# Kernel tuning notes

Hardware: AMD Instinct MI355X
Metric: run time of the kernel (lower is better)

The kernel has to match this reference:

```python
import jax, jax.numpy as jnp
import numpy as np

B, N_SRC, N_TGT = 2, 2048, 2048
DIM, HEADS, DIM_HEAD, DIM_ROT = 1024, 16, 64, 32
INNER = HEADS * DIM_HEAD
SCALE = DIM_HEAD ** -0.5


def rotate_every_two(x):
    # (..., d) with d even: pairs (x1, x2) -> (-x2, x1), interleaved
    x1 = x[..., ::2]
    x2 = x[..., 1::2]
    return jnp.stack((-x2, x1), axis=-1).reshape(x.shape)


def setup_inputs() -> dict:
    key = jax.random.key(0)
    ks = jax.random.split(key, 10)
    return {
        "src": jax.random.normal(ks[0], (B, N_SRC, DIM), jnp.float32),
        "sin_src": jax.random.uniform(ks[1], (B, N_SRC, DIM_ROT), jnp.float32, -1.0, 1.0),
        "cos_src": jax.random.uniform(ks[2], (B, N_SRC, DIM_ROT), jnp.float32, -1.0, 1.0),
        "tgt": jax.random.normal(ks[3], (B, N_TGT, DIM), jnp.float32),
        "sin_tgt": jax.random.uniform(ks[4], (B, N_TGT, DIM_ROT), jnp.float32, -1.0, 1.0),
        "cos_tgt": jax.random.uniform(ks[5], (B, N_TGT, DIM_ROT), jnp.float32, -1.0, 1.0),
        "wq": jax.random.normal(ks[6], (DIM, INNER), jnp.float32) / np.sqrt(DIM),
        "wkv": jax.random.normal(ks[7], (DIM, 2 * INNER), jnp.float32) / np.sqrt(DIM),
        "wout": jax.random.normal(ks[8], (INNER, DIM), jnp.float32) / np.sqrt(INNER),
        "bout": jnp.zeros((DIM,), jnp.float32),
    }


def reference(src, sin_src, cos_src, tgt, sin_tgt, cos_tgt, wq, wkv, wout, bout):
    b = src.shape[0]
    q = tgt @ wq                                  # (b, i, inner)
    k, v = jnp.split(src @ wkv, 2, axis=-1)       # (b, j, inner) each

    def split_heads(t):
        return t.reshape(b, t.shape[1], HEADS, DIM_HEAD).transpose(0, 2, 1, 3)

    q, k, v = map(split_heads, (q, k, v))          # (b, h, n, d)

    # rotary on leading DIM_ROT dims; pos embs broadcast across heads
    st, ct = sin_tgt[:, None], cos_tgt[:, None]    # (b, 1, i, dr)
    ss, cs = sin_src[:, None], cos_src[:, None]    # (b, 1, j, dr)
    q_rot, q_pass = q[..., :DIM_ROT], q[..., DIM_ROT:]
    k_rot, k_pass = k[..., :DIM_ROT], k[..., DIM_ROT:]
    q_rot = q_rot * ct + rotate_every_two(q_rot) * st
    k_rot = k_rot * cs + rotate_every_two(k_rot) * ss
    q = jnp.concatenate([q_rot, q_pass], axis=-1)
    k = jnp.concatenate([k_rot, k_pass], axis=-1)

    dots = jnp.einsum('bhid,bhjd->bhij', q, k) * SCALE
    attn = jax.nn.softmax(dots, axis=-1)
    out = jnp.einsum('bhij,bhjd->bhid', attn, v)
    out = out.transpose(0, 2, 1, 3).reshape(b, out.shape[2], INNER)
    return out @ wout + bout, attn
```

## Files before the change

kernel.cpp:

```cpp
#include <hip/hip_runtime.h>
#include <hip/hip_bf16.h>
#include <cstdint>
#include <cstddef>

#define NB 2
#define NSEQ 2048
#define NHEADS 16
#define HD 64
#define DMODEL 1024
#define SCALEF 0.125f

typedef __attribute__((ext_vector_type(4))) float f32x4;
typedef __attribute__((ext_vector_type(8))) short s16x8;

__device__ __forceinline__ unsigned short f2bf(float f) {
  union { float f; unsigned u; } v; v.f = f;
  unsigned u = v.u;
  return (unsigned short)((u + 0x7fffu + ((u >> 16) & 1u)) >> 16);
}
__device__ __forceinline__ float bf2f(unsigned short s) {
  union { unsigned u; float f; } v; v.u = ((unsigned)s) << 16;
  return v.f;
}

__global__ void k_convert(const float* __restrict__ in, unsigned short* __restrict__ out, int n4) {
  int i = blockIdx.x * blockDim.x + threadIdx.x;
  if (i >= n4) return;
  float4 v = ((const float4*)in)[i];
  ushort4 o;
  o.x = f2bf(v.x); o.y = f2bf(v.y); o.z = f2bf(v.z); o.w = f2bf(v.w);
  ((ushort4*)out)[i] = o;
}

__global__ void k_transpose(const float* __restrict__ w, unsigned short* __restrict__ wt, int K, int N) {
  __shared__ float t[64][65];
  int n0 = blockIdx.x * 64, k0 = blockIdx.y * 64;
  int c = threadIdx.x & 63, rb = threadIdx.x >> 6;
#pragma unroll
  for (int rr = 0; rr < 16; rr++) {
    int k = rb * 16 + rr;
    t[c][k] = w[(size_t)(k0 + k) * N + n0 + c];
  }
  __syncthreads();
#pragma unroll
  for (int rr = 0; rr < 16; rr++) {
    int n = rb * 16 + rr;
    wt[(size_t)(n0 + n) * K + k0 + c] = f2bf(t[n][c]);
  }
}

#define GLD16(gp, lp) __builtin_amdgcn_global_load_lds( \
    (const __attribute__((address_space(1))) unsigned int*)(gp), \
    (__attribute__((address_space(3))) unsigned int*)(lp), 16, 0, 0)

__global__ __launch_bounds__(256) void k_gemm(const unsigned short* __restrict__ A,
                                              const unsigned short* __restrict__ Bt,
                                              float* __restrict__ C,
                                              const float* __restrict__ bias,
                                              int M, int N, int K) {
  __shared__ unsigned short As[128 * 32];
  __shared__ unsigned short Bs[128 * 32];
  const int tid = threadIdx.x;
  const int lane = tid & 63, wid = tid >> 6;
  const int m0 = blockIdx.y * 128, n0 = blockIdx.x * 128;
  const int wr = wid >> 1, wc = wid & 1;
  const int lr = lane >> 2, l4 = lane & 3;
  const int lc = lane & 15, lg = lane >> 4;

  const unsigned short* pa0 = A + (size_t)(m0 + wid * 32 + lr) * K + l4 * 8;
  const unsigned short* pa1 = pa0 + (size_t)16 * K;
  const unsigned short* pb0 = Bt + (size_t)(n0 + wid * 32 + lr) * K + l4 * 8;
  const unsigned short* pb1 = pb0 + (size_t)16 * K;

  f32x4 acc[4][4] = {};

  for (int kt = 0; kt < K; kt += 32) {
    GLD16(pa0 + kt, &As[wid * 1024]);
    GLD16(pa1 + kt, &As[wid * 1024 + 512]);
    GLD16(pb0 + kt, &Bs[wid * 1024]);
    GLD16(pb1 + kt, &Bs[wid * 1024 + 512]);
    __syncthreads();
    s16x8 af[4], bfr[4];
#pragma unroll
    for (int m = 0; m < 4; m++)
      af[m] = *(const s16x8*)&As[(wr * 64 + m * 16 + lc) * 32 + lg * 8];
#pragma unroll
    for (int n = 0; n < 4; n++)
      bfr[n] = *(const s16x8*)&Bs[(wc * 64 + n * 16 + lc) * 32 + lg * 8];
    __builtin_amdgcn_s_setprio(1);
#pragma unroll
    for (int m = 0; m < 4; m++)
#pragma unroll
      for (int n = 0; n < 4; n++)
        acc[m][n] = __builtin_amdgcn_mfma_f32_16x16x32_bf16(af[m], bfr[n], acc[m][n], 0, 0, 0);
    __builtin_amdgcn_s_setprio(0);
    __syncthreads();
  }

  float bv[4] = {0.f, 0.f, 0.f, 0.f};
  if (bias) {
#pragma unroll
    for (int n = 0; n < 4; n++) bv[n] = bias[n0 + wc * 64 + n * 16 + lc];
  }
#pragma unroll
  for (int m = 0; m < 4; m++) {
#pragma unroll
    for (int n = 0; n < 4; n++) {
      int col = n0 + wc * 64 + n * 16 + lc;
#pragma unroll
      for (int r = 0; r < 4; r++) {
        int row = m0 + wr * 64 + m * 16 + lg * 4 + r;
        C[(size_t)row * N + col] = acc[m][n][r] + bv[n];
      }
    }
  }
}

__global__ void k_rope(const float* __restrict__ src, int row_stride,
                       const float* __restrict__ sinp, const float* __restrict__ cosp,
                       unsigned short* __restrict__ dst) {
  int tid = blockIdx.x * 256 + threadIdx.x;
  int p = tid & 31;
  int h = (tid >> 5) & 15;
  int i = (tid >> 9) & 2047;
  int b = tid >> 20;
  int d = p * 2;
  float2 x = *(const float2*)(src + (size_t)(b * NSEQ + i) * row_stride + h * HD + d);
  float o0, o1;
  if (p < 16) {
    size_t sc = (size_t)(b * NSEQ + i) * 32 + d;
    float2 cc = *(const float2*)(cosp + sc);
    float2 ss = *(const float2*)(sinp + sc);
    o0 = x.x * cc.x - x.y * ss.x;
    o1 = x.y * cc.y + x.x * ss.y;
  } else { o0 = x.x; o1 = x.y; }
  size_t off = ((size_t)(b * NHEADS + h) * NSEQ + i) * HD + d;
  unsigned pack = (unsigned)f2bf(o0) | ((unsigned)f2bf(o1) << 16);
  *(unsigned*)(dst + off) = pack;
}

__global__ void k_vtrans(const float* __restrict__ kv, unsigned short* __restrict__ vt) {
  __shared__ float t[64][65];
  int i0 = blockIdx.x * 64;
  int h = blockIdx.y, b = blockIdx.z;
  int c = threadIdx.x & 63, rb = threadIdx.x >> 6;
#pragma unroll
  for (int rr = 0; rr < 16; rr++) {
    int il = rb * 16 + rr;
    t[il][c] = kv[(size_t)(b * NSEQ + i0 + il) * 2048 + 1024 + h * HD + c];
  }
  __syncthreads();
#pragma unroll
  for (int rr = 0; rr < 16; rr++) {
    int dd = rb * 16 + rr;
    vt[((size_t)(b * NHEADS + h) * HD + dd) * NSEQ + i0 + c] = f2bf(t[c][dd]);
  }
}

#define QBLK 32
#define SROWB 2056
__global__ __launch_bounds__(1024, 4) void k_attn(const unsigned short* __restrict__ qh,
                                                  const unsigned short* __restrict__ kh,
                                                  const unsigned short* __restrict__ vt,
                                                  float* __restrict__ attn_g,
                                                  unsigned short* __restrict__ ctx) {
  __shared__ unsigned short Sbf[QBLK * SROWB];
  __shared__ float wred[16][32];
  __shared__ float invr[32];
  float* part = (float*)Sbf;

  const int tid = threadIdx.x;
  const int lane = tid & 63, wid = tid >> 6;
  const int i0 = blockIdx.x * QBLK;
  const int h = blockIdx.y, b = blockIdx.z;
  const int lc = lane & 15, lg = lane >> 4;
  const int wcb = wid * 128;

  const unsigned short* qb = qh + ((size_t)(b * NHEADS + h) * NSEQ + i0) * HD;
  const unsigned short* kb = kh + (size_t)(b * NHEADS + h) * NSEQ * HD;
  const unsigned short* vb = vt + (size_t)(b * NHEADS + h) * HD * NSEQ;

  s16x8 aq[2][2];
#pragma unroll
  for (int rg = 0; rg < 2; rg++) {
    aq[rg][0] = *(const s16x8*)&qb[(rg * 16 + lc) * HD + lg * 8];
    aq[rg][1] = *(const s16x8*)&qb[(rg * 16 + lc) * HD + 32 + lg * 8];
  }
  float psum[2][4] = {};
  const unsigned short* krow = kb + (size_t)(wcb + lc) * HD + lg * 8;
  s16x8 kp[2][2];
  kp[0][0] = *(const s16x8*)&krow[0];
  kp[0][1] = *(const s16x8*)&krow[32];
#pragma unroll
  for (int jf = 0; jf < 8; jf++) {
    if (jf < 7) {
      kp[(jf + 1) & 1][0] = *(const s16x8*)&krow[(size_t)((jf + 1) * 16) * HD];
      kp[(jf + 1) & 1][1] = *(const s16x8*)&krow[(size_t)((jf + 1) * 16) * HD + 32];
    }
    int j = wcb + jf * 16;
#pragma unroll
    for (int rg = 0; rg < 2; rg++) {
      f32x4 acc = {};
      acc = __builtin_amdgcn_mfma_f32_16x16x32_bf16(aq[rg][0], kp[jf & 1][0], acc, 0, 0, 0);
      acc = __builtin_amdgcn_mfma_f32_16x16x32_bf16(aq[rg][1], kp[jf & 1][1], acc, 0, 0, 0);
#pragma unroll
      for (int r = 0; r < 4; r++) {
        float e = __expf(acc[r] * SCALEF);
        psum[rg][r] += e;
        Sbf[(size_t)(rg * 16 + lg * 4 + r) * SROWB + j + lc] = f2bf(e);
      }
    }
  }
#pragma unroll
  for (int off = 1; off <= 8; off <<= 1)
#pragma unroll
    for (int rg = 0; rg < 2; rg++)
#pragma unroll
      for (int r = 0; r < 4; r++) psum[rg][r] += __shfl_xor(psum[rg][r], off);
  if (lc == 0) {
#pragma unroll
    for (int rg = 0; rg < 2; rg++)
#pragma unroll
      for (int r = 0; r < 4; r++) wred[wid][rg * 16 + lg * 4 + r] = psum[rg][r];
  }
  __syncthreads();
  if (tid < 32) {
    float tot = 0.f;
#pragma unroll
    for (int w = 0; w < 16; w++) tot += wred[w][tid];
    invr[tid] = 1.0f / tot;
  }

  f32x4 accd[2][4] = {};
  const unsigned short* vrow = vb + (size_t)lc * NSEQ + wcb + lg * 8;
  s16x8 vp[2][4];
#pragma unroll
  for (int f = 0; f < 4; f++)
    vp[0][f] = *(const s16x8*)&vrow[(size_t)(f * 16) * NSEQ];
#pragma unroll
  for (int jj = 0; jj < 4; jj++) {
    if (jj < 3) {
#pragma unroll
      for (int f = 0; f < 4; f++)
        vp[(jj + 1) & 1][f] = *(const s16x8*)&vrow[(size_t)(f * 16) * NSEQ + (jj + 1) * 32];
    }
    int jb = wcb + jj * 32;
    s16x8 af0 = *(const s16x8*)&Sbf[(size_t)lc * SROWB + jb + lg * 8];
    __builtin_amdgcn_s_setprio(1);
#pragma unroll
    for (int f = 0; f < 4; f++)
      accd[0][f] = __builtin_amdgcn_mfma_f32_16x16x32_bf16(af0, vp[jj & 1][f], accd[0][f], 0, 0, 0);
    __builtin_amdgcn_s_setprio(0);
    s16x8 af1 = *(const s16x8*)&Sbf[(size_t)(16 + lc) * SROWB + jb + lg * 8];
    __builtin_amdgcn_s_setprio(1);
#pragma unroll
    for (int f = 0; f < 4; f++)
      accd[1][f] = __builtin_amdgcn_mfma_f32_16x16x32_bf16(af1, vp[jj & 1][f], accd[1][f], 0, 0, 0);
    __builtin_amdgcn_s_setprio(0);
  }
  __syncthreads();

  {
    const int srow = tid >> 5;
    const int scc = (tid & 31) * 8;
    const float inv = invr[srow];
    float* arow = attn_g + ((size_t)(b * NHEADS + h) * NSEQ + i0 + srow) * NSEQ + scc;
#pragma unroll
    for (int k = 0; k < 8; k++) {
      s16x8 ev = *(const s16x8*)&Sbf[(size_t)srow * SROWB + scc + k * 256];
      f32x4 f0, f1;
      f0[0] = bf2f((unsigned short)ev[0]) * inv;
      f0[1] = bf2f((unsigned short)ev[1]) * inv;
      f0[2] = bf2f((unsigned short)ev[2]) * inv;
      f0[3] = bf2f((unsigned short)ev[3]) * inv;
      f1[0] = bf2f((unsigned short)ev[4]) * inv;
      f1[1] = bf2f((unsigned short)ev[5]) * inv;
      f1[2] = bf2f((unsigned short)ev[6]) * inv;
      f1[3] = bf2f((unsigned short)ev[7]) * inv;
      *(f32x4*)&arow[k * 256] = f0;
      *(f32x4*)&arow[k * 256 + 4] = f1;
    }
  }
  __syncthreads();

  if (wid < 8) {
#pragma unroll
    for (int rg = 0; rg < 2; rg++)
#pragma unroll
      for (int f = 0; f < 4; f++)
#pragma unroll
        for (int r = 0; r < 4; r++)
          part[((size_t)wid * 32 + rg * 16 + lg * 4 + r) * 65 + f * 16 + lc] = accd[rg][f][r];
  }
  __syncthreads();
  if (wid >= 8) {
#pragma unroll
    for (int rg = 0; rg < 2; rg++)
#pragma unroll
      for (int f = 0; f < 4; f++)
#pragma unroll
        for (int r = 0; r < 4; r++)
          part[((size_t)(wid - 8) * 32 + rg * 16 + lg * 4 + r) * 65 + f * 16 + lc] += accd[rg][f][r];
  }
  __syncthreads();

  {
    const int oi = tid >> 5;
    const int d0 = (tid & 31) * 2;
    float s0 = 0.f, s1 = 0.f;
#pragma unroll
    for (int p = 0; p < 8; p++) {
      s0 += part[((size_t)p * 32 + oi) * 65 + d0];
      s1 += part[((size_t)p * 32 + oi) * 65 + d0 + 1];
    }
    float iv = invr[oi];
    ushort2 o;
    o.x = f2bf(s0 * iv);
    o.y = f2bf(s1 * iv);
    *(ushort2*)&ctx[(size_t)(b * NSEQ + i0 + oi) * DMODEL + h * HD + d0] = o;
  }
}

extern "C" void kernel_launch(void* const* d_in, const int* in_sizes, int n_in,
                              void* d_out, int out_size, void* d_ws, size_t ws_size,
                              hipStream_t stream) {
  const float* src     = (const float*)d_in[0];
  const float* sin_src = (const float*)d_in[1];
  const float* cos_src = (const float*)d_in[2];
  const float* tgt     = (const float*)d_in[3];
  const float* sin_tgt = (const float*)d_in[4];
  const float* cos_tgt = (const float*)d_in[5];
  const float* wq      = (const float*)d_in[6];
  const float* wkv     = (const float*)d_in[7];
  const float* wout    = (const float*)d_in[8];
  const float* bout    = (const float*)d_in[9];

  if (ws_size < (size_t)109051904) return;

  uint8_t* w = (uint8_t*)d_ws;
  unsigned short* tgt_bf = (unsigned short*)(w + 0);
  unsigned short* src_bf = (unsigned short*)(w + 8388608);
  unsigned short* wq_t   = (unsigned short*)(w + 16777216);
  unsigned short* wkv_t  = (unsigned short*)(w + 18874368);
  unsigned short* wout_t = (unsigned short*)(w + 23068672);
  float*          q_ws   = (float*)(w + 25165824);
  float*          kv_ws  = (float*)(w + 41943040);
  unsigned short* qhb    = (unsigned short*)(w + 75497472);
  unsigned short* khb    = (unsigned short*)(w + 83886080);
  unsigned short* vtb    = (unsigned short*)(w + 92274688);
  unsigned short* ctx    = (unsigned short*)(w + 100663296);

  float* out_p  = (float*)d_out;
  float* attn_p = out_p + (size_t)NB * NSEQ * DMODEL;

  k_convert<<<4096, 256, 0, stream>>>(tgt, tgt_bf, 1048576);
  k_convert<<<4096, 256, 0, stream>>>(src, src_bf, 1048576);
  k_transpose<<<dim3(16, 16), 256, 0, stream>>>(wq,   wq_t,   1024, 1024);
  k_transpose<<<dim3(32, 16), 256, 0, stream>>>(wkv,  wkv_t,  1024, 2048);
  k_transpose<<<dim3(16, 16), 256, 0, stream>>>(wout, wout_t, 1024, 1024);

  k_gemm<<<dim3(8, 32),  256, 0, stream>>>(tgt_bf, wq_t,  q_ws,  nullptr, 4096, 1024, 1024);
  k_gemm<<<dim3(16, 32), 256, 0, stream>>>(src_bf, wkv_t, kv_ws, nullptr, 4096, 2048, 1024);

  k_rope<<<8192, 256, 0, stream>>>(q_ws, 1024, sin_tgt, cos_tgt, qhb);
  k_rope<<<8192, 256, 0, stream>>>(kv_ws, 2048, sin_src, cos_src, khb);
  k_vtrans<<<dim3(32, 16, 2), 256, 0, stream>>>(kv_ws, vtb);

  k_attn<<<dim3(64, 16, 2), 1024, 0, stream>>>(qhb, khb, vtb, attn_p, ctx);

  k_gemm<<<dim3(8, 32), 256, 0, stream>>>(ctx, wout_t, out_p, bout, 4096, 1024, 1024);
}
```

Before: 390.0 us.

## Fuse rope and V-transpose into projection GEMM epilogues, merge prep launches

The Q and KV projection GEMMs now apply rotary embedding in their epilogues, using lane shuffles for the pair partner, and write bf16 head-major Q/K and transposed V directly. This removes the fp32 intermediate buffers and the separate rope and V-transpose kernels. The two input conversions are merged into one launch, and the three weight transposes into another, to cut launch overhead. Risks include scattered 2-byte epilogue stores and extra sin/cos global loads per output element.

```diff
diff --git a/kernel.cpp b/kernel.cpp
--- a/kernel.cpp
+++ b/kernel.cpp
@@ -23,16 +23,27 @@
   return v.f;
 }
 
-__global__ void k_convert(const float* __restrict__ in, unsigned short* __restrict__ out, int n4) {
-  int i = blockIdx.x * blockDim.x + threadIdx.x;
-  if (i >= n4) return;
+__global__ void k_convert2(const float* __restrict__ a, const float* __restrict__ b,
+                           unsigned short* __restrict__ oa, unsigned short* __restrict__ ob) {
+  int bx = blockIdx.x;
+  const float* in = (bx < 4096) ? a : b;
+  unsigned short* out = (bx < 4096) ? oa : ob;
+  int i = (bx & 4095) * 256 + threadIdx.x;
   float4 v = ((const float4*)in)[i];
   ushort4 o;
   o.x = f2bf(v.x); o.y = f2bf(v.y); o.z = f2bf(v.z); o.w = f2bf(v.w);
   ((ushort4*)out)[i] = o;
 }
 
-__global__ void k_transpose(const float* __restrict__ w, unsigned short* __restrict__ wt, int K, int N) {
+__global__ void k_transpose_all(const float* __restrict__ wq, unsigned short* __restrict__ wq_t,
+                                const float* __restrict__ wkv, unsigned short* __restrict__ wkv_t,
+                                const float* __restrict__ wout, unsigned short* __restrict__ wout_t) {
+  const int z = blockIdx.z;
+  const float* w; unsigned short* wt; int N;
+  if (z == 0)      { w = wq;   wt = wq_t;   N = 1024; }
+  else if (z == 1) { w = wkv;  wt = wkv_t;  N = 2048; }
+  else             { w = wout; wt = wout_t; N = 1024; }
+  if (blockIdx.x * 64 >= N) return;
   __shared__ float t[64][65];
   int n0 = blockIdx.x * 64, k0 = blockIdx.y * 64;
   int c = threadIdx.x & 63, rb = threadIdx.x >> 6;
@@ -45,7 +56,7 @@
 #pragma unroll
   for (int rr = 0; rr < 16; rr++) {
     int n = rb * 16 + rr;
-    wt[(size_t)(n0 + n) * K + k0 + c] = f2bf(t[n][c]);
+    wt[(size_t)(n0 + n) * 1024 + k0 + c] = f2bf(t[n][c]);
   }
 }
 
@@ -53,55 +64,51 @@
     (const __attribute__((address_space(1))) unsigned int*)(gp), \
     (__attribute__((address_space(3))) unsigned int*)(lp), 16, 0, 0)
 
+#define GEMM_BODY(A, Bt)                                                        \
+  __shared__ unsigned short As[128 * 32];                                       \
+  __shared__ unsigned short Bs[128 * 32];                                       \
+  const int tid = threadIdx.x;                                                  \
+  const int lane = tid & 63, wid = tid >> 6;                                    \
+  const int m0 = blockIdx.y * 128, n0 = blockIdx.x * 128;                       \
+  const int wr = wid >> 1, wc = wid & 1;                                        \
+  const int lr = lane >> 2, l4 = lane & 3;                                      \
+  const int lc = lane & 15, lg = lane >> 4;                                     \
+  const unsigned short* pa0 = A + (size_t)(m0 + wid * 32 + lr) * 1024 + l4 * 8; \
+  const unsigned short* pa1 = pa0 + (size_t)16 * 1024;                          \
+  const unsigned short* pb0 = Bt + (size_t)(n0 + wid * 32 + lr) * 1024 + l4 * 8;\
+  const unsigned short* pb1 = pb0 + (size_t)16 * 1024;                          \
+  f32x4 acc[4][4] = {};                                                         \
+  for (int kt = 0; kt < 1024; kt += 32) {                                       \
+    GLD16(pa0 + kt, &As[wid * 1024]);                                           \
+    GLD16(pa1 + kt, &As[wid * 1024 + 512]);                                     \
+    GLD16(pb0 + kt, &Bs[wid * 1024]);                                           \
+    GLD16(pb1 + kt, &Bs[wid * 1024 + 512]);                                     \
+    __syncthreads();                                                            \
+    s16x8 af[4], bfr[4];                                                        \
+    _Pragma("unroll")                                                           \
+    for (int m = 0; m < 4; m++)                                                 \
+      af[m] = *(const s16x8*)&As[(wr * 64 + m * 16 + lc) * 32 + lg * 8];        \
+    _Pragma("unroll")                                                           \
+    for (int n = 0; n < 4; n++)                                                 \
+      bfr[n] = *(const s16x8*)&Bs[(wc * 64 + n * 16 + lc) * 32 + lg * 8];       \
+    __builtin_amdgcn_s_setprio(1);                                              \
+    _Pragma("unroll")                                                           \
+    for (int m = 0; m < 4; m++)                                                 \
+      _Pragma("unroll")                                                         \
+      for (int n = 0; n < 4; n++)                                               \
+        acc[m][n] = __builtin_amdgcn_mfma_f32_16x16x32_bf16(af[m], bfr[n], acc[m][n], 0, 0, 0); \
+    __builtin_amdgcn_s_setprio(0);                                              \
+    __syncthreads();                                                            \
+  }
+
 __global__ __launch_bounds__(256) void k_gemm(const unsigned short* __restrict__ A,
                                               const unsigned short* __restrict__ Bt,
                                               float* __restrict__ C,
-                                              const float* __restrict__ bias,
-                                              int M, int N, int K) {
-  __shared__ unsigned short As[128 * 32];
-  __shared__ unsigned short Bs[128 * 32];
-  const int tid = threadIdx.x;
-  const int lane = tid & 63, wid = tid >> 6;
-  const int m0 = blockIdx.y * 128, n0 = blockIdx.x * 128;
-  const int wr = wid >> 1, wc = wid & 1;
-  const int lr = lane >> 2, l4 = lane & 3;
-  const int lc = lane & 15, lg = lane >> 4;
-
-  const unsigned short* pa0 = A + (size_t)(m0 + wid * 32 + lr) * K + l4 * 8;
-  const unsigned short* pa1 = pa0 + (size_t)16 * K;
-  const unsigned short* pb0 = Bt + (size_t)(n0 + wid * 32 + lr) * K + l4 * 8;
-  const unsigned short* pb1 = pb0 + (size_t)16 * K;
-
-  f32x4 acc[4][4] = {};
-
-  for (int kt = 0; kt < K; kt += 32) {
-    GLD16(pa0 + kt, &As[wid * 1024]);
-    GLD16(pa1 + kt, &As[wid * 1024 + 512]);
-    GLD16(pb0 + kt, &Bs[wid * 1024]);
-    GLD16(pb1 + kt, &Bs[wid * 1024 + 512]);
-    __syncthreads();
-    s16x8 af[4], bfr[4];
-#pragma unroll
-    for (int m = 0; m < 4; m++)
-      af[m] = *(const s16x8*)&As[(wr * 64 + m * 16 + lc) * 32 + lg * 8];
-#pragma unroll
-    for (int n = 0; n < 4; n++)
-      bfr[n] = *(const s16x8*)&Bs[(wc * 64 + n * 16 + lc) * 32 + lg * 8];
-    __builtin_amdgcn_s_setprio(1);
-#pragma unroll
-    for (int m = 0; m < 4; m++)
-#pragma unroll
-      for (int n = 0; n < 4; n++)
-        acc[m][n] = __builtin_amdgcn_mfma_f32_16x16x32_bf16(af[m], bfr[n], acc[m][n], 0, 0, 0);
-    __builtin_amdgcn_s_setprio(0);
-    __syncthreads();
-  }
-
-  float bv[4] = {0.f, 0.f, 0.f, 0.f};
-  if (bias) {
-#pragma unroll
-    for (int n = 0; n < 4; n++) bv[n] = bias[n0 + wc * 64 + n * 16 + lc];
-  }
+                                              const float* __restrict__ bias) {
+  GEMM_BODY(A, Bt)
+  float bv[4];
+#pragma unroll
+  for (int n = 0; n < 4; n++) bv[n] = bias[n0 + wc * 64 + n * 16 + lc];
 #pragma unroll
   for (int m = 0; m < 4; m++) {
 #pragma unroll
@@ -110,50 +117,85 @@
 #pragma unroll
       for (int r = 0; r < 4; r++) {
         int row = m0 + wr * 64 + m * 16 + lg * 4 + r;
-        C[(size_t)row * N + col] = acc[m][n][r] + bv[n];
+        C[(size_t)row * 1024 + col] = acc[m][n][r] + bv[n];
       }
     }
   }
 }
 
-__global__ void k_rope(const float* __restrict__ src, int row_stride,
-                       const float* __restrict__ sinp, const float* __restrict__ cosp,
-                       unsigned short* __restrict__ dst) {
-  int tid = blockIdx.x * 256 + threadIdx.x;
-  int p = tid & 31;
-  int h = (tid >> 5) & 15;
-  int i = (tid >> 9) & 2047;
-  int b = tid >> 20;
-  int d = p * 2;
-  float2 x = *(const float2*)(src + (size_t)(b * NSEQ + i) * row_stride + h * HD + d);
-  float o0, o1;
-  if (p < 16) {
-    size_t sc = (size_t)(b * NSEQ + i) * 32 + d;
-    float2 cc = *(const float2*)(cosp + sc);
-    float2 ss = *(const float2*)(sinp + sc);
-    o0 = x.x * cc.x - x.y * ss.x;
-    o1 = x.y * cc.y + x.x * ss.y;
-  } else { o0 = x.x; o1 = x.y; }
-  size_t off = ((size_t)(b * NHEADS + h) * NSEQ + i) * HD + d;
-  unsigned pack = (unsigned)f2bf(o0) | ((unsigned)f2bf(o1) << 16);
-  *(unsigned*)(dst + off) = pack;
-}
-
-__global__ void k_vtrans(const float* __restrict__ kv, unsigned short* __restrict__ vt) {
-  __shared__ float t[64][65];
-  int i0 = blockIdx.x * 64;
-  int h = blockIdx.y, b = blockIdx.z;
-  int c = threadIdx.x & 63, rb = threadIdx.x >> 6;
-#pragma unroll
-  for (int rr = 0; rr < 16; rr++) {
-    int il = rb * 16 + rr;
-    t[il][c] = kv[(size_t)(b * NSEQ + i0 + il) * 2048 + 1024 + h * HD + c];
-  }
-  __syncthreads();
-#pragma unroll
-  for (int rr = 0; rr < 16; rr++) {
-    int dd = rb * 16 + rr;
-    vt[((size_t)(b * NHEADS + h) * HD + dd) * NSEQ + i0 + c] = f2bf(t[c][dd]);
+__global__ __launch_bounds__(256) void k_gemmq(const unsigned short* __restrict__ A,
+                                               const unsigned short* __restrict__ Bt,
+                                               const float* __restrict__ sinp,
+                                               const float* __restrict__ cosp,
+                                               unsigned short* __restrict__ qhb) {
+  GEMM_BODY(A, Bt)
+#pragma unroll
+  for (int m = 0; m < 4; m++) {
+#pragma unroll
+    for (int n = 0; n < 4; n++) {
+      int c = n0 + wc * 64 + n * 16 + lc;
+      int h = c >> 6, d = c & 63;
+      bool dorope = (d < 32);
+#pragma unroll
+      for (int r = 0; r < 4; r++) {
+        int row = m0 + wr * 64 + m * 16 + lg * 4 + r;
+        float x = acc[m][n][r];
+        float px = __shfl_xor(x, 1);
+        float o = x;
+        if (dorope) {
+          float s = sinp[(size_t)row * 32 + d];
+          float cz = cosp[(size_t)row * 32 + d];
+          o = (d & 1) ? (x * cz + px * s) : (x * cz - px * s);
+        }
+        int b = row >> 11, i = row & 2047;
+        qhb[((size_t)(b * NHEADS + h) * NSEQ + i) * HD + d] = f2bf(o);
+      }
+    }
+  }
+}
+
+__global__ __launch_bounds__(256) void k_gemmkv(const unsigned short* __restrict__ A,
+                                                const unsigned short* __restrict__ Bt,
+                                                const float* __restrict__ sinp,
+                                                const float* __restrict__ cosp,
+                                                unsigned short* __restrict__ khb,
+                                                unsigned short* __restrict__ vtb) {
+  GEMM_BODY(A, Bt)
+#pragma unroll
+  for (int m = 0; m < 4; m++) {
+#pragma unroll
+    for (int n = 0; n < 4; n++) {
+      int c = n0 + wc * 64 + n * 16 + lc;
+      int d = c & 63;
+      if (c < 1024) {
+        int h = c >> 6;
+        bool dorope = (d < 32);
+#pragma unroll
+        for (int r = 0; r < 4; r++) {
+          int row = m0 + wr * 64 + m * 16 + lg * 4 + r;
+          float x = acc[m][n][r];
+          float px = __shfl_xor(x, 1);
+          float o = x;
+          if (dorope) {
+            float s = sinp[(size_t)row * 32 + d];
+            float cz = cosp[(size_t)row * 32 + d];
+            o = (d & 1) ? (x * cz + px * s) : (x * cz - px * s);
+          }
+          int b = row >> 11, i = row & 2047;
+          khb[((size_t)(b * NHEADS + h) * NSEQ + i) * HD + d] = f2bf(o);
+        }
+      } else {
+        int h = (c - 1024) >> 6;
+#pragma unroll
+        for (int r = 0; r < 4; r++) (void)__shfl_xor(acc[m][n][r], 1);
+        ushort4 o;
+        o.x = f2bf(acc[m][n][0]); o.y = f2bf(acc[m][n][1]);
+        o.z = f2bf(acc[m][n][2]); o.w = f2bf(acc[m][n][3]);
+        int row0 = m0 + wr * 64 + m * 16 + lg * 4;
+        int b = row0 >> 11, i = row0 & 2047;
+        *(ushort4*)&vtb[((size_t)(b * NHEADS + h) * HD + d) * NSEQ + i] = o;
+      }
+    }
   }
 }
 
@@ -343,8 +385,6 @@
   unsigned short* wq_t   = (unsigned short*)(w + 16777216);
   unsigned short* wkv_t  = (unsigned short*)(w + 18874368);
   unsigned short* wout_t = (unsigned short*)(w + 23068672);
-  float*          q_ws   = (float*)(w + 25165824);
-  float*          kv_ws  = (float*)(w + 41943040);
   unsigned short* qhb    = (unsigned short*)(w + 75497472);
   unsigned short* khb    = (unsigned short*)(w + 83886080);
   unsigned short* vtb    = (unsigned short*)(w + 92274688);
@@ -353,20 +393,13 @@
   float* out_p  = (float*)d_out;
   float* attn_p = out_p + (size_t)NB * NSEQ * DMODEL;
 
-  k_convert<<<4096, 256, 0, stream>>>(tgt, tgt_bf, 1048576);
-  k_convert<<<4096, 256, 0, stream>>>(src, src_bf, 1048576);
-  k_transpose<<<dim3(16, 16), 256, 0, stream>>>(wq,   wq_t,   1024, 1024);
-  k_transpose<<<dim3(32, 16), 256, 0, stream>>>(wkv,  wkv_t,  1024, 2048);
-  k_transpose<<<dim3(16, 16), 256, 0, stream>>>(wout, wout_t, 1024, 1024);
-
-  k_gemm<<<dim3(8, 32),  256, 0, stream>>>(tgt_bf, wq_t,  q_ws,  nullptr, 4096, 1024, 1024);
-  k_gemm<<<dim3(16, 32), 256, 0, stream>>>(src_bf, wkv_t, kv_ws, nullptr, 4096, 2048, 1024);
-
-  k_rope<<<8192, 256, 0, stream>>>(q_ws, 1024, sin_tgt, cos_tgt, qhb);
-  k_rope<<<8192, 256, 0, stream>>>(kv_ws, 2048, sin_src, cos_src, khb);
-  k_vtrans<<<dim3(32, 16, 2), 256, 0, stream>>>(kv_ws, vtb);
+  k_convert2<<<8192, 256, 0, stream>>>(tgt, src, tgt_bf, src_bf);
+  k_transpose_all<<<dim3(32, 16, 3), 256, 0, stream>>>(wq, wq_t, wkv, wkv_t, wout, wout_t);
+
+  k_gemmq <<<dim3(8, 32),  256, 0, stream>>>(tgt_bf, wq_t,  sin_tgt, cos_tgt, qhb);
+  k_gemmkv<<<dim3(16, 32), 256, 0, stream>>>(src_bf, wkv_t, sin_src, cos_src, khb, vtb);
 
   k_attn<<<dim3(64, 16, 2), 1024, 0, stream>>>(qhb, khb, vtb, attn_p, ctx);
 
-  k_gemm<<<dim3(8, 32), 256, 0, stream>>>(ctx, wout_t, out_p, bout, 4096, 1024, 1024);
-}
+  k_gemm<<<dim3(8, 32), 256, 0, stream>>>(ctx, wout_t, out_p, bout);
+}
```

Measured after the change: 358.8 us. 8.0% less time.
